# Kernel optimization log

Measured on AMD Instinct MI355X. Metric: run time of the kernel, lower is better.

Reference implementation:

```python
import jax, jax.numpy as jnp
import numpy as np
import math

T, B, D = 2048, 4, 1024
H, HD = 16, 64  # num_heads, head_dim


def _rope_cos_sin(t_len, head_dim):
    inv_freq = 1.0 / (10000.0 ** (jnp.arange(0, head_dim, 2, dtype=jnp.float32) / head_dim))
    t = jnp.arange(t_len, dtype=jnp.float32)
    freqs = jnp.einsum('i,j->ij', t, inv_freq)          # (T, HD/2)
    emb = jnp.concatenate([freqs, freqs], axis=-1)       # (T, HD)
    # broadcast over (T, B, H, HD)
    return jnp.cos(emb)[:, None, None, :], jnp.sin(emb)[:, None, None, :]


def _rotate_half(x):
    x1, x2 = jnp.split(x, 2, axis=-1)
    return jnp.concatenate([-x2, x1], axis=-1)


def setup_inputs() -> dict:
    key = jax.random.key(0)
    ks = jax.random.split(key, 5)
    x = jax.random.normal(ks[0], (T, B, D), dtype=jnp.float32)
    # causal mask: True = masked (future positions), shape (T, T)
    attention_mask = jnp.triu(jnp.ones((T, T), dtype=bool), k=1)
    W_qkv = jax.random.normal(ks[1], (3 * D, D), dtype=jnp.float32) * (1.0 / math.sqrt(D))
    b_qkv = jax.random.normal(ks[2], (3 * D,), dtype=jnp.float32) * 0.02
    W_out = jax.random.normal(ks[3], (D, D), dtype=jnp.float32) * (1.0 / math.sqrt(D))
    b_out = jax.random.normal(ks[4], (D,), dtype=jnp.float32) * 0.02
    return {"x": x, "attention_mask": attention_mask, "W_qkv": W_qkv,
            "b_qkv": b_qkv, "W_out": W_out, "b_out": b_out}


def reference(x, attention_mask, W_qkv, b_qkv, W_out, b_out):
    t_len, b_sz, d = x.shape
    qkv = x @ W_qkv.T + b_qkv                              # (T, B, 3D)
    q, k, v = jnp.split(qkv, 3, axis=-1)
    q = q.reshape(t_len, b_sz, H, HD)
    k = k.reshape(t_len, b_sz, H, HD)
    v = v.reshape(t_len, b_sz, H, HD)

    cos, sin = _rope_cos_sin(t_len, HD)
    q = q * cos + _rotate_half(q) * sin
    k = k * cos + _rotate_half(k) * sin

    scale = math.sqrt(HD)
    # scores: (B, H, T, S)
    scores = jnp.einsum('tbhd,sbhd->bhts', q, k) / scale
    scores = jnp.where(attention_mask[None, None, :, :], -jnp.inf, scores)
    probs = jax.nn.softmax(scores.astype(jnp.float32), axis=-1).astype(v.dtype)
    context = jnp.einsum('bhts,sbhd->tbhd', probs, v)      # (T, B, H, HD)
    context = context.reshape(t_len, b_sz, d)
    return context @ W_out.T + b_out
```

## Files before the change

### kernel.cpp

```cpp
#include <hip/hip_runtime.h>
#include <math.h>

#define T_LEN 2048
#define B_SZ 4
#define D_MODEL 1024
#define NH 16
#define HD 64
#define BH_TOT (B_SZ*NH)

typedef __attribute__((ext_vector_type(8))) short bf16x8;
typedef __attribute__((ext_vector_type(4))) float f32x4;
typedef __attribute__((ext_vector_type(16))) float f32x16;
typedef __attribute__((ext_vector_type(8))) unsigned short u16x8;
typedef __attribute__((ext_vector_type(4))) unsigned short u16x4;

union U8 { unsigned int u[4]; bf16x8 v; };

static __device__ __forceinline__ unsigned short f2bf(float f) {
  unsigned int x = __float_as_uint(f);
  x += 0x7fffu + ((x >> 16) & 1u);
  return (unsigned short)(x >> 16);
}
static __device__ __forceinline__ float bf2f(unsigned short u) {
  return __uint_as_float(((unsigned int)u) << 16);
}
static __device__ __forceinline__ void gload16(const void* g, void* l) {
  __builtin_amdgcn_global_load_lds((const __attribute__((address_space(1))) void*)g,
                                   (__attribute__((address_space(3))) void*)l, 16, 0, 0);
}

#define QS_SCALE 0.18033688011112042f

__global__ __launch_bounds__(256) void cvt3_kernel(
    const float* __restrict__ x, const float* __restrict__ wq, const float* __restrict__ wo,
    unsigned short* __restrict__ xb, unsigned short* __restrict__ wqb,
    unsigned short* __restrict__ wob, float2* __restrict__ tab) {
  const int i = blockIdx.x * 256 + threadIdx.x;
  const int N1 = T_LEN * B_SZ * D_MODEL / 8;
  const int N2 = N1 + 3 * D_MODEL * D_MODEL / 8;
  const int N3 = N2 + D_MODEL * D_MODEL / 8;
  if (i >= N3) {
    const int j = i - N3;
    if (j < T_LEN * 32) {
      const int t = j >> 5, fi = j & 31;
      const float inv_freq = powf(10000.f, -(float)fi / 32.f);
      float s, c;
      sincosf((float)t * inv_freq, &s, &c);
      tab[j] = make_float2(c, s);
    }
    return;
  }
  const float* s; unsigned short* d; int off;
  if (i < N1)      { s = x;  d = xb;  off = i; }
  else if (i < N2) { s = wq; d = wqb; off = i - N1; }
  else             { s = wo; d = wob; off = i - N2; }
  const float4 a = ((const float4*)s)[off * 2];
  const float4 b = ((const float4*)s)[off * 2 + 1];
  u16x8 o;
  o[0] = f2bf(a.x); o[1] = f2bf(a.y); o[2] = f2bf(a.z); o[3] = f2bf(a.w);
  o[4] = f2bf(b.x); o[5] = f2bf(b.y); o[6] = f2bf(b.z); o[7] = f2bf(b.w);
  ((u16x8*)d)[off] = o;
}

__global__ __launch_bounds__(256, 4) void gemm_mfma_kernel(
    const unsigned short* __restrict__ A, const unsigned short* __restrict__ W,
    const float* __restrict__ bias, float* __restrict__ C,
    int M, int N, int K, int mode,
    unsigned short* __restrict__ qd, unsigned short* __restrict__ kd,
    unsigned short* __restrict__ vtd, const float2* __restrict__ tab)
{
  __shared__ unsigned short As[128 * 64];
  __shared__ unsigned short Bs[128 * 64];
  const int tid = threadIdx.x;
  const int l = tid & 63, w = tid >> 6;
  const int lq = l & 15, lg = l >> 4;
  const int wm = w >> 1, wn = w & 1;
  const int m0 = blockIdx.x * 128, n0 = blockIdx.y * 128;

  const int lrow = l >> 3;
  const int lcolb = ((l & 7) << 4) ^ (lrow << 4);

  f32x4 acc[4][4];
#pragma unroll
  for (int mt = 0; mt < 4; ++mt)
#pragma unroll
    for (int nt = 0; nt < 4; ++nt)
#pragma unroll
      for (int r2 = 0; r2 < 4; ++r2) acc[mt][nt][r2] = 0.f;

  for (int k0 = 0; k0 < K; k0 += 64) {
    __syncthreads();
#pragma unroll
    for (int c = 0; c < 4; ++c) {
      const int r0 = w * 32 + c * 8;
      const int row = r0 + lrow;
      gload16((const char*)A + ((size_t)(m0 + row) * K + k0) * 2 + lcolb,
              (char*)As + r0 * 128);
      gload16((const char*)W + ((size_t)(n0 + row) * K + k0) * 2 + lcolb,
              (char*)Bs + r0 * 128);
    }
    __syncthreads();

#pragma unroll
    for (int kc = 0; kc < 2; ++kc) {
      bf16x8 af[4], bfr[4];
#pragma unroll
      for (int mt = 0; mt < 4; ++mt) {
        const int r = wm * 64 + mt * 16 + lq;
        af[mt] = *(const bf16x8*)((const char*)As + r * 128 +
                                  ((kc * 64 + lg * 16) ^ ((r & 7) << 4)));
      }
#pragma unroll
      for (int nt = 0; nt < 4; ++nt) {
        const int r = wn * 64 + nt * 16 + lq;
        bfr[nt] = *(const bf16x8*)((const char*)Bs + r * 128 +
                                   ((kc * 64 + lg * 16) ^ ((r & 7) << 4)));
      }
#pragma unroll
      for (int mt = 0; mt < 4; ++mt)
#pragma unroll
        for (int nt = 0; nt < 4; ++nt)
          acc[mt][nt] = __builtin_amdgcn_mfma_f32_16x16x32_bf16(af[mt], bfr[nt], acc[mt][nt], 0, 0, 0);
    }
  }

  if (mode == 0) {
#pragma unroll
    for (int nt = 0; nt < 4; ++nt) {
      const int n = n0 + wn * 64 + nt * 16 + lq;
      const float bv = bias[n];
#pragma unroll
      for (int mt = 0; mt < 4; ++mt)
#pragma unroll
        for (int r2 = 0; r2 < 4; ++r2) {
          const int m = m0 + wm * 64 + mt * 16 + lg * 4 + r2;
          C[(size_t)m * N + n] = acc[mt][nt][r2] + bv;
        }
    }
  } else {
    const int nb = n0 + wn * 64;
    const int which = nb >> 10;
    const int h = (nb >> 6) & (NH - 1);
    float bv[4];
#pragma unroll
    for (int nt = 0; nt < 4; ++nt) bv[nt] = bias[nb + nt * 16 + lq];

    if (which == 2) {
#pragma unroll
      for (int nt = 0; nt < 4; ++nt) {
        const int hd = nt * 16 + lq;
#pragma unroll
        for (int mt = 0; mt < 4; ++mt) {
          const int mbase = m0 + wm * 64 + mt * 16;
          const int t = (mbase >> 2) + lg;
#pragma unroll
          for (int r2 = 0; r2 < 4; ++r2) {
            const int b = r2;
            vtd[((size_t)(b * NH + h) * HD + hd) * T_LEN + t] =
                f2bf(acc[mt][nt][r2] + bv[nt]);
          }
        }
      }
    } else {
      unsigned short* dst = (which == 0) ? qd : kd;
      const float sc = (which == 0) ? QS_SCALE : 1.0f;
#pragma unroll
      for (int mt = 0; mt < 4; ++mt) {
        const int mbase = m0 + wm * 64 + mt * 16;
        const int t = (mbase >> 2) + lg;
        const float2 cs0 = tab[t * 32 + lq];
        const float2 cs1 = tab[t * 32 + 16 + lq];
#pragma unroll
        for (int r2 = 0; r2 < 4; ++r2) {
          const int b = r2;
          const float v0 = acc[mt][0][r2] + bv[0];
          const float v1 = acc[mt][1][r2] + bv[1];
          const float v2 = acc[mt][2][r2] + bv[2];
          const float v3 = acc[mt][3][r2] + bv[3];
          const float o0 = (v0 * cs0.x - v2 * cs0.y) * sc;
          const float o2 = (v2 * cs0.x + v0 * cs0.y) * sc;
          const float o1 = (v1 * cs1.x - v3 * cs1.y) * sc;
          const float o3 = (v3 * cs1.x + v1 * cs1.y) * sc;
          unsigned short* p = dst + ((size_t)(b * NH + h) * T_LEN + t) * HD;
          p[lq]      = f2bf(o0);
          p[16 + lq] = f2bf(o1);
          p[32 + lq] = f2bf(o2);
          p[48 + lq] = f2bf(o3);
        }
      }
    }
  }
}

__global__ __launch_bounds__(256, 4) void attn_mfma_kernel(
    const unsigned short* __restrict__ Qb,
    const unsigned short* __restrict__ Kb,
    const unsigned short* __restrict__ Vt,
    unsigned short* __restrict__ ctx)
{
  __shared__ unsigned short Ks[2][64 * 64];
  __shared__ unsigned short Vs[2][64 * 64];
  const int tid = threadIdx.x;
  const int l = tid & 63;
  const int w = tid >> 6;
  const int lq = l & 31;
  const int h = l >> 5;
  const int bh = blockIdx.x;
  const int qc = (T_LEN / 128 - 1) - blockIdx.y;
  const int b = bh >> 4, hh = bh & 15;
  const size_t tb = (size_t)bh * T_LEN;

  const int q0w = qc * 128 + w * 32;
  const int qg = q0w + lq;

  bf16x8 qf[4];
#pragma unroll
  for (int s = 0; s < 4; ++s)
    qf[s] = *(const bf16x8*)(Qb + (tb + qg) * HD + s * 16 + h * 8);

  f32x16 acc0, acc1;
#pragma unroll
  for (int r = 0; r < 16; ++r) { acc0[r] = 0.f; acc1[r] = 0.f; }
  float mrun = -1e30f, lsum = 0.f;

  const int lrow = l >> 3;
  const int lcolb = ((l & 7) << 4) ^ (lrow << 4);
  const int last = 2 * qc + 1;

#pragma unroll
  for (int c = 0; c < 2; ++c) {
    const int r0 = w * 16 + c * 8;
    const int row = r0 + lrow;
    gload16((const char*)Kb + ((tb + row) * HD) * 2 + lcolb, (char*)Ks[0] + r0 * 128);
    gload16((const char*)Vt + (((size_t)bh * HD + row) * T_LEN) * 2 + lcolb,
            (char*)Vs[0] + r0 * 128);
  }
  __syncthreads();

  for (int kbi = 0; kbi <= last; ++kbi) {
    const int s0 = kbi * 64;
    const int cur = kbi & 1;

    if (kbi < last) {
      const int sn = s0 + 64;
#pragma unroll
      for (int c = 0; c < 2; ++c) {
        const int r0 = w * 16 + c * 8;
        const int row = r0 + lrow;
        gload16((const char*)Kb + ((tb + sn + row) * HD) * 2 + lcolb,
                (char*)Ks[cur ^ 1] + r0 * 128);
        gload16((const char*)Vt + (((size_t)bh * HD + row) * T_LEN + sn) * 2 + lcolb,
                (char*)Vs[cur ^ 1] + r0 * 128);
      }
    }

    const int dmax = q0w + 31 - s0;
    if (dmax >= 0) {
      const char* Kc = (const char*)Ks[cur];
      const char* Vc = (const char*)Vs[cur];
      const bool st1 = (dmax >= 32);
      const bool maskN = (s0 + 63 > q0w);

      f32x16 sv0, sv1;
#pragma unroll
      for (int r = 0; r < 16; ++r) { sv0[r] = -1e30f; sv1[r] = -1e30f; }
      {
        f32x16 z;
#pragma unroll
        for (int r = 0; r < 16; ++r) z[r] = 0.f;
        const int krow = lq;
        const int kswz = (krow & 7) << 4;
        __builtin_amdgcn_s_setprio(1);
#pragma unroll
        for (int s = 0; s < 4; ++s) {
          bf16x8 ka = *(const bf16x8*)(Kc + krow * 128 + ((s * 32 + h * 16) ^ kswz));
          z = __builtin_amdgcn_mfma_f32_32x32x16_bf16(ka, qf[s], z, 0, 0, 0);
        }
        __builtin_amdgcn_s_setprio(0);
        sv0 = z;
      }
      if (st1) {
        f32x16 z;
#pragma unroll
        for (int r = 0; r < 16; ++r) z[r] = 0.f;
        const int krow = 32 + lq;
        const int kswz = (krow & 7) << 4;
        __builtin_amdgcn_s_setprio(1);
#pragma unroll
        for (int s = 0; s < 4; ++s) {
          bf16x8 ka = *(const bf16x8*)(Kc + krow * 128 + ((s * 32 + h * 16) ^ kswz));
          z = __builtin_amdgcn_mfma_f32_32x32x16_bf16(ka, qf[s], z, 0, 0, 0);
        }
        __builtin_amdgcn_s_setprio(0);
        sv1 = z;
      }

      if (maskN) {
#pragma unroll
        for (int r = 0; r < 16; ++r) {
          const int sl = (r & 3) + 8 * (r >> 2) + 4 * h;
          if (s0 + sl > qg)      sv0[r] = -1e30f;
          if (s0 + 32 + sl > qg) sv1[r] = -1e30f;
        }
      }

      float pm[4];
#pragma unroll
      for (int j = 0; j < 4; ++j) pm[j] = fmaxf(sv0[j], sv1[j]);
#pragma unroll
      for (int r = 4; r < 16; ++r) pm[r & 3] = fmaxf(pm[r & 3], fmaxf(sv0[r], sv1[r]));
      float pmax = fmaxf(fmaxf(pm[0], pm[1]), fmaxf(pm[2], pm[3]));
      pmax = fmaxf(pmax, __shfl_xor(pmax, 32));

      if (!__all(pmax - mrun <= 8.0f)) {
        const float mnew = fmaxf(mrun, pmax);
        const float alpha = exp2f(mrun - mnew);
        lsum *= alpha;
#pragma unroll
        for (int r = 0; r < 16; ++r) { acc0[r] *= alpha; acc1[r] *= alpha; }
        mrun = mnew;
      }

      float s4[4] = {0.f, 0.f, 0.f, 0.f};
#pragma unroll
      for (int r = 0; r < 16; ++r) { sv0[r] = exp2f(sv0[r] - mrun); s4[r & 3] += sv0[r]; }
      if (st1) {
#pragma unroll
        for (int r = 0; r < 16; ++r) { sv1[r] = exp2f(sv1[r] - mrun); s4[r & 3] += sv1[r]; }
      }
      float ps = (s4[0] + s4[1]) + (s4[2] + s4[3]);
      ps += __shfl_xor(ps, 32);
      lsum += ps;

      unsigned int u0[4][2], u1[4][2];
#pragma unroll
      for (int a = 0; a < 4; ++a) {
        asm("v_cvt_pk_bf16_f32 %0, %1, %2" : "=v"(u0[a][0]) : "v"(sv0[4*a]),   "v"(sv0[4*a+1]));
        asm("v_cvt_pk_bf16_f32 %0, %1, %2" : "=v"(u0[a][1]) : "v"(sv0[4*a+2]), "v"(sv0[4*a+3]));
      }
      if (st1) {
#pragma unroll
        for (int a = 0; a < 4; ++a) {
          asm("v_cvt_pk_bf16_f32 %0, %1, %2" : "=v"(u1[a][0]) : "v"(sv1[4*a]),   "v"(sv1[4*a+1]));
          asm("v_cvt_pk_bf16_f32 %0, %1, %2" : "=v"(u1[a][1]) : "v"(sv1[4*a+2]), "v"(sv1[4*a+3]));
        }
      }

      const int vswz0 = (lq & 7) << 4;
#pragma unroll
      for (int st = 0; st < 2; ++st) {
        if (st == 1 && !st1) break;
#pragma unroll
        for (int cc = 0; cc < 2; ++cc) {
          unsigned int x0 = st ? u1[2*cc][0] : u0[2*cc][0];
          unsigned int y0 = st ? u1[2*cc+1][0] : u0[2*cc+1][0];
          unsigned int x1 = st ? u1[2*cc][1] : u0[2*cc][1];
          unsigned int y1 = st ? u1[2*cc+1][1] : u0[2*cc+1][1];
          asm("v_permlane32_swap_b32 %0, %1" : "+v"(x0), "+v"(y0));
          asm("v_permlane32_swap_b32 %0, %1" : "+v"(x1), "+v"(y1));
          U8 pf;
          pf.u[0] = x0; pf.u[1] = x1; pf.u[2] = y0; pf.u[3] = y1;
          const int soff = st * 64 + cc * 32 + h * 16;
          __builtin_amdgcn_s_setprio(1);
          {
            bf16x8 va = *(const bf16x8*)(Vc + lq * 128 + (soff ^ vswz0));
            acc0 = __builtin_amdgcn_mfma_f32_32x32x16_bf16(va, pf.v, acc0, 0, 0, 0);
          }
          {
            const int row = 32 + lq;
            bf16x8 va = *(const bf16x8*)(Vc + row * 128 + (soff ^ ((row & 7) << 4)));
            acc1 = __builtin_amdgcn_mfma_f32_32x32x16_bf16(va, pf.v, acc1, 0, 0, 0);
          }
          __builtin_amdgcn_s_setprio(0);
        }
      }
    }

    __syncthreads();
  }

  const float linv = 1.f / lsum;
  unsigned short* orow = ctx + ((size_t)qg * B_SZ + b) * D_MODEL + hh * HD;
#pragma unroll
  for (int g = 0; g < 4; ++g) {
    u16x4 o0, o1;
#pragma unroll
    for (int j = 0; j < 4; ++j) {
      o0[j] = f2bf(acc0[4*g + j] * linv);
      o1[j] = f2bf(acc1[4*g + j] * linv);
    }
    *(u16x4*)(orow + 8*g + 4*h)      = o0;
    *(u16x4*)(orow + 32 + 8*g + 4*h) = o1;
  }
}

extern "C" void kernel_launch(void* const* d_in, const int* in_sizes, int n_in,
                              void* d_out, int out_size, void* d_ws, size_t ws_size,
                              hipStream_t stream) {
  const float* x    = (const float*)d_in[0];
  const float* Wqkv = (const float*)d_in[2];
  const float* bqkv = (const float*)d_in[3];
  const float* Wout = (const float*)d_in[4];
  const float* bout = (const float*)d_in[5];
  float* out = (float*)d_out;

  char* wsb = (char*)d_ws;
  unsigned short* xb    = (unsigned short*)(wsb);
  unsigned short* wqkvb = (unsigned short*)(wsb + (16ull << 20));
  unsigned short* woutb = (unsigned short*)(wsb + (22ull << 20));
  unsigned short* qb    = (unsigned short*)(wsb + (24ull << 20));
  unsigned short* kb    = (unsigned short*)(wsb + (40ull << 20));
  unsigned short* vt    = (unsigned short*)(wsb + (56ull << 20));
  unsigned short* ctxb  = (unsigned short*)(wsb + (72ull << 20));
  float2* tab           = (float2*)(wsb + (88ull << 20));

  const int ncvt = T_LEN*B_SZ*D_MODEL/8 + 3*D_MODEL*D_MODEL/8 + D_MODEL*D_MODEL/8
                 + T_LEN * 32;
  cvt3_kernel<<<(ncvt + 255)/256, 256, 0, stream>>>(x, Wqkv, Wout, xb, wqkvb, woutb, tab);

  dim3 g1((T_LEN * B_SZ) / 128, 3 * D_MODEL / 128);
  gemm_mfma_kernel<<<g1, 256, 0, stream>>>(xb, wqkvb, bqkv, nullptr,
                                           T_LEN * B_SZ, 3 * D_MODEL, D_MODEL, 1,
                                           qb, kb, vt, tab);

  dim3 g2(BH_TOT, T_LEN / 128);
  attn_mfma_kernel<<<g2, 256, 0, stream>>>(qb, kb, vt, ctxb);

  dim3 g3((T_LEN * B_SZ) / 128, D_MODEL / 128);
  gemm_mfma_kernel<<<g3, 256, 0, stream>>>(ctxb, woutb, bout, out,
                                           T_LEN * B_SZ, D_MODEL, D_MODEL, 0,
                                           nullptr, nullptr, nullptr, tab);
}
```

Before: 185.3 us.

## Double-buffer LDS tiles in MFMA GEMM to overlap global loads with compute

The GEMM kernel now keeps two LDS buffers for A and W tiles and prefetches two K-steps ahead using direct-to-LDS loads. It replaces the per-iteration __syncthreads pair with partial vmcnt waits and raw barriers, so global memory latency overlaps MFMA work. The cost is doubled LDS use (64KB per block), and launch bounds are lowered to 2 blocks per CU, so occupancy falls. The hand-written vmcnt count also depends on exactly 8 outstanding loads per stage.

```diff
diff --git a/kernel.cpp b/kernel.cpp
--- a/kernel.cpp
+++ b/kernel.cpp
@@ -62,15 +62,15 @@
   ((u16x8*)d)[off] = o;
 }
 
-__global__ __launch_bounds__(256, 4) void gemm_mfma_kernel(
+__global__ __launch_bounds__(256, 2) void gemm_mfma_kernel(
     const unsigned short* __restrict__ A, const unsigned short* __restrict__ W,
     const float* __restrict__ bias, float* __restrict__ C,
     int M, int N, int K, int mode,
     unsigned short* __restrict__ qd, unsigned short* __restrict__ kd,
     unsigned short* __restrict__ vtd, const float2* __restrict__ tab)
 {
-  __shared__ unsigned short As[128 * 64];
-  __shared__ unsigned short Bs[128 * 64];
+  __shared__ unsigned short As[2][128 * 64];
+  __shared__ unsigned short Bs[2][128 * 64];
   const int tid = threadIdx.x;
   const int l = tid & 63, w = tid >> 6;
   const int lq = l & 15, lg = l >> 4;
@@ -88,18 +88,27 @@
 #pragma unroll
       for (int r2 = 0; r2 < 4; ++r2) acc[mt][nt][r2] = 0.f;
 
-  for (int k0 = 0; k0 < K; k0 += 64) {
-    __syncthreads();
+  const int nk = K >> 6;
+  auto stage = [&](int kt, int buf) {
 #pragma unroll
     for (int c = 0; c < 4; ++c) {
       const int r0 = w * 32 + c * 8;
       const int row = r0 + lrow;
-      gload16((const char*)A + ((size_t)(m0 + row) * K + k0) * 2 + lcolb,
-              (char*)As + r0 * 128);
-      gload16((const char*)W + ((size_t)(n0 + row) * K + k0) * 2 + lcolb,
-              (char*)Bs + r0 * 128);
-    }
-    __syncthreads();
+      gload16((const char*)A + ((size_t)(m0 + row) * K + kt * 64) * 2 + lcolb,
+              (char*)As[buf] + r0 * 128);
+      gload16((const char*)W + ((size_t)(n0 + row) * K + kt * 64) * 2 + lcolb,
+              (char*)Bs[buf] + r0 * 128);
+    }
+  };
+
+  stage(0, 0);
+  stage(1, 1);
+
+  for (int kt = 0; kt < nk; ++kt) {
+    const int cur = kt & 1;
+    if (kt + 1 < nk) { asm volatile("s_waitcnt vmcnt(8)" ::: "memory"); }
+    else             { asm volatile("s_waitcnt vmcnt(0)" ::: "memory"); }
+    __builtin_amdgcn_s_barrier();
 
 #pragma unroll
     for (int kc = 0; kc < 2; ++kc) {
@@ -107,13 +116,13 @@
 #pragma unroll
       for (int mt = 0; mt < 4; ++mt) {
         const int r = wm * 64 + mt * 16 + lq;
-        af[mt] = *(const bf16x8*)((const char*)As + r * 128 +
+        af[mt] = *(const bf16x8*)((const char*)As[cur] + r * 128 +
                                   ((kc * 64 + lg * 16) ^ ((r & 7) << 4)));
       }
 #pragma unroll
       for (int nt = 0; nt < 4; ++nt) {
         const int r = wn * 64 + nt * 16 + lq;
-        bfr[nt] = *(const bf16x8*)((const char*)Bs + r * 128 +
+        bfr[nt] = *(const bf16x8*)((const char*)Bs[cur] + r * 128 +
                                    ((kc * 64 + lg * 16) ^ ((r & 7) << 4)));
       }
 #pragma unroll
@@ -122,6 +131,10 @@
         for (int nt = 0; nt < 4; ++nt)
           acc[mt][nt] = __builtin_amdgcn_mfma_f32_16x16x32_bf16(af[mt], bfr[nt], acc[mt][nt], 0, 0, 0);
     }
+
+    asm volatile("" ::: "memory");
+    __builtin_amdgcn_s_barrier();
+    if (kt + 2 < nk) stage(kt + 2, cur);
   }
 
   if (mode == 0) {
```

Measured after the change: 179.5 us (median of 2 runs). 1.03x faster.
